# Kernel optimization log

Hardware: AMD Instinct MI355X
Metric: run time of the kernel (lower is better)

## Reference

```python
import jax, jax.numpy as jnp
import numpy as np

N_NODES = 100000
N_EDGES = 3200000
IN_DIM = 256
EMB_DIM = 64
BATCH = 4096
WEIGHT_DECAY = 1e-4


def setup_inputs() -> dict:
    key = jax.random.key(0)
    ks = jax.random.split(key, 8)
    feats = jax.random.normal(ks[0], (N_NODES, IN_DIM), dtype=jnp.float32)
    W = jax.random.normal(ks[1], (IN_DIM, EMB_DIM), dtype=jnp.float32) * (1.0 / np.sqrt(IN_DIM))
    edge_row = jax.random.randint(ks[2], (N_EDGES,), 0, N_NODES, dtype=jnp.int32)
    edge_col = jax.random.randint(ks[3], (N_EDGES,), 0, N_NODES, dtype=jnp.int32)
    edge_val = jax.random.uniform(ks[4], (N_EDGES,), dtype=jnp.float32) * 0.05  # normalized adj weights
    idx1 = jax.random.randint(ks[5], (BATCH,), 0, N_NODES, dtype=jnp.int32)
    idx2 = jax.random.randint(ks[6], (BATCH,), 0, N_NODES, dtype=jnp.int32)
    neg_idx = jax.random.randint(ks[7], (BATCH,), 0, N_NODES, dtype=jnp.int32)
    return {"feats": feats, "W": W, "edge_row": edge_row, "edge_col": edge_col,
            "edge_val": edge_val, "idx1": idx1, "idx2": idx2, "neg_idx": neg_idx}


def reference(feats, W, edge_row, edge_col, edge_val, idx1, idx2, neg_idx):
    # GraphConvolution: tanh( A_sparse @ (X @ W) ), A in COO form
    xw = feats @ W                                              # [N, D]
    msgs = edge_val[:, None] * xw[edge_col]                     # [E, D] gather + scale
    h = jax.ops.segment_sum(msgs, edge_row, num_segments=N_NODES)  # sparse-dense matmul
    h = jnp.tanh(h)
    # tf.nn.l2_normalize(embedding, 1)
    sq = jnp.sum(h * h, axis=1, keepdims=True)
    emb = h * jax.lax.rsqrt(jnp.maximum(sq, 1e-12))             # [N, D]
    # embedding lookups
    o1, o2, on = emb[idx1], emb[idx2], emb[neg_idx]             # [B, D] each
    y_ui = jnp.sum(o1 * o2, axis=1)
    y_uj = jnp.sum(o1 * on, axis=1)
    # BPR loss + weight decay (tf.nn.l2_loss = 0.5*sum(x^2))
    bpr = jnp.sum(-jax.nn.log_sigmoid(y_ui - y_uj))
    loss = (bpr + WEIGHT_DECAY * 0.5 * jnp.sum(emb * emb)) / jnp.float32(BATCH)
    return loss
```

## Files before the change

### kernel.cpp

```cpp
#include <hip/hip_runtime.h>
#include <cmath>

#define N_NODES 100000
#define N_EDGES 3200000
#define IN_DIM 256
#define EMB 64
#define BATCH 4096
#define MWAVES 6250
#define NBUCK 782
#define BROWS 128
#define BSTRIDE 4608
#define PSTRIDE 5504
#define EPB 12544
#define NPA 256

typedef unsigned long long u64;
typedef unsigned int u32;
typedef unsigned short u16;
typedef __attribute__((ext_vector_type(8))) short bf16x8;
typedef __attribute__((ext_vector_type(4))) float f32x4;

__device__ __forceinline__ float wave_sum(float v) {
#pragma unroll
    for (int m = 1; m < 64; m <<= 1) v += __shfl_xor(v, m, 64);
    return v;
}

__device__ __forceinline__ u16 f2bf_rne(float f) {
    u32 u = __float_as_uint(f);
    u32 r = ((u >> 16) & 1u) + 0x7FFFu;
    return (u16)((u + r) >> 16);
}

__device__ __forceinline__ float bf2f(u32 bits16) {
    return __uint_as_float(bits16 << 16);
}

__global__ __launch_bounds__(256) void wpack_kernel(const float* __restrict__ W,
                                                    u16* __restrict__ wpack) {
    const int idx = blockIdx.x * 256 + threadIdx.x;
    const int f = idx >> 6, lane = idx & 63;
    const int kt = f >> 2, nt = f & 3;
    const int k0 = kt * 32 + (lane >> 4) * 8;
    const int n  = nt * 16 + (lane & 15);
    u32 buf[4];
#pragma unroll
    for (int jj = 0; jj < 4; ++jj) {
        u16 lo = f2bf_rne(W[(size_t)(k0 + 2 * jj) * EMB + n]);
        u16 hi = f2bf_rne(W[(size_t)(k0 + 2 * jj + 1) * EMB + n]);
        buf[jj] = (u32)lo | ((u32)hi << 16);
    }
    *(uint4*)&wpack[idx * 8] = *(uint4*)buf;
}

__global__ __launch_bounds__(256) void mfma_gemm_kernel(const float* __restrict__ feats,
                                                        const u16* __restrict__ wpack,
                                                        u16* __restrict__ xwb) {
    __shared__ u16 wlds[32 * 64 * 8];
    const int tid = threadIdx.x;
    for (int idx = tid; idx < 32 * 64; idx += 256)
        *(uint4*)&wlds[idx * 8] = *(const uint4*)&wpack[idx * 8];
    __syncthreads();

    const int wave = tid >> 6, lane = tid & 63;
    const int wid = blockIdx.x * 4 + wave;
    if (wid >= MWAVES) return;
    const int row0 = wid * 16;
    const int arow = row0 + (lane & 15);
    const int kbase = (lane >> 4) * 8;
    const float* fr = feats + (size_t)arow * IN_DIM + kbase;

    float4 av[16];
#pragma unroll
    for (int kt = 0; kt < 8; ++kt) {
        av[2 * kt]     = *(const float4*)(fr + kt * 32);
        av[2 * kt + 1] = *(const float4*)(fr + kt * 32 + 4);
    }

    f32x4 acc[4] = {};
    const u16* wl = &wlds[lane * 8];
#pragma unroll
    for (int kt = 0; kt < 8; ++kt) {
        float4 a0 = av[2 * kt], a1 = av[2 * kt + 1];
        u32 ab[4];
        ab[0] = (u32)f2bf_rne(a0.x) | ((u32)f2bf_rne(a0.y) << 16);
        ab[1] = (u32)f2bf_rne(a0.z) | ((u32)f2bf_rne(a0.w) << 16);
        ab[2] = (u32)f2bf_rne(a1.x) | ((u32)f2bf_rne(a1.y) << 16);
        ab[3] = (u32)f2bf_rne(a1.z) | ((u32)f2bf_rne(a1.w) << 16);
        bf16x8 afrag = *(bf16x8*)ab;
#pragma unroll
        for (int nt = 0; nt < 4; ++nt) {
            bf16x8 bfrag = *(const bf16x8*)&wl[(kt * 4 + nt) * 512];
            acc[nt] = __builtin_amdgcn_mfma_f32_16x16x32_bf16(afrag, bfrag, acc[nt], 0, 0, 0);
        }
    }
    const int rb = row0 + (lane >> 4) * 4;
    const int cb = lane & 15;
#pragma unroll
    for (int nt = 0; nt < 4; ++nt)
#pragma unroll
        for (int r = 0; r < 4; ++r)
            xwb[(size_t)(rb + r) * EMB + nt * 16 + cb] = f2bf_rne(acc[nt][r]);
}

__global__ __launch_bounds__(1024, 4) void passA_kernel(const int* __restrict__ erow,
                                                        const int* __restrict__ ecol,
                                                        const float* __restrict__ eval,
                                                        u32* __restrict__ gcursor,
                                                        u64* __restrict__ sorted) {
    __shared__ u64 stage[EPB];
    __shared__ u32 hist[1024];
    __shared__ u32 harr[1024];
    __shared__ u32 cursor[1024];
    __shared__ u32 gbase[1024];

    const int tid = threadIdx.x;
    const int e0 = blockIdx.x * EPB;
    const int total = min(EPB, N_EDGES - e0);

    hist[tid] = 0;
    __syncthreads();

    u64 ent[13];
#pragma unroll
    for (int j = 0; j < 13; ++j) {
        const int le = j * 1024 + tid;
        if (le < total) {
            const int e = e0 + le;
            const int r = erow[e];
            const int c = ecol[e];
            const u16 vb = f2bf_rne(eval[e]);
            ent[j] = (u64)(u32)r | ((u64)(u32)c << 17) | ((u64)vb << 34);
            atomicAdd(&hist[r >> 7], 1u);
        }
    }
    __syncthreads();

    const u32 h = hist[tid];
    harr[tid] = h;
    __syncthreads();
    for (int off = 1; off < 1024; off <<= 1) {
        u32 x = (tid >= off) ? harr[tid - off] : 0;
        __syncthreads();
        harr[tid] += x;
        __syncthreads();
    }
    const u32 myoff = harr[tid] - h;
    __syncthreads();
    harr[tid] = myoff;
    cursor[tid] = myoff;
    gbase[tid] = h ? atomicAdd(&gcursor[tid], h) : 0u;
    __syncthreads();

#pragma unroll
    for (int j = 0; j < 13; ++j) {
        const int le = j * 1024 + tid;
        if (le < total) {
            const u64 p = ent[j];
            const u32 pos = atomicAdd(&cursor[(int)(p & 0x1FFFFu) >> 7], 1u);
            stage[pos] = p;
        }
    }
    __syncthreads();

    for (int i = tid; i < total; i += 1024) {
        const u64 p = stage[i];
        const int bk = (int)(p & 0x1FFFFu) >> 7;
        const u32 gpos = gbase[bk] + ((u32)i - harr[bk]);
        if (gpos < BSTRIDE) sorted[(size_t)bk * BSTRIDE + gpos] = p;
    }
}

__global__ __launch_bounds__(512, 4) void gather_kernel(const u16* __restrict__ xwb,
                                                        u64* __restrict__ sorted,
                                                        const u32* __restrict__ gcursor,
                                                        float* __restrict__ accumA) {
    __shared__ u32 scoff[PSTRIDE];
    __shared__ u16 sval[PSTRIDE];
    __shared__ u32 rhist[BROWS], roff[BROWS], rcur[BROWS], sc[BROWS];
    __shared__ float part[8];
    const int tid = threadIdx.x, wave = tid >> 6, lane = tid & 63;
    const int b = blockIdx.x;
    u64* gbase = sorted + (size_t)b * BSTRIDE;
    const int cnt = min((int)gcursor[b], BSTRIDE);

    if (tid < BROWS) rhist[tid] = 0;
    __syncthreads();

    u64 ent[9];
    int nloc = 0;
    for (int i = tid; i < cnt; i += 512) {
        u64 p = gbase[i];
        ent[nloc++] = p;
        atomicAdd(&rhist[(int)(p & 127u)], 1u);
    }
    __syncthreads();

    if (tid < BROWS) sc[tid] = (rhist[tid] + 7u) & ~7u;
    __syncthreads();
    for (int off = 1; off < BROWS; off <<= 1) {
        u32 x = (tid < BROWS && tid >= off) ? sc[tid - off] : 0;
        __syncthreads();
        if (tid < BROWS) sc[tid] += x;
        __syncthreads();
    }
    if (tid < BROWS) {
        const u32 r0 = sc[tid] - ((rhist[tid] + 7u) & ~7u);
        roff[tid] = r0;
        rcur[tid] = r0;
    }
    __syncthreads();

    for (int j = 0; j < nloc; ++j) {
        const u64 p = ent[j];
        const u32 pos = atomicAdd(&rcur[(int)(p & 127u)], 1u);
        scoff[pos] = (((u32)(p >> 17)) & 0x1FFFFu) << 7;
        sval[pos]  = (u16)(p >> 34);
    }
    __syncthreads();

    if (tid < BROWS) {
        const int e = roff[tid] + rhist[tid];
        const int pe = roff[tid] + (int)((rhist[tid] + 7u) & ~7u);
        for (int k = e; k < pe; ++k) { scoff[k] = 0u; sval[k] = 0; }
    }
    __syncthreads();

    u16* embp = (u16*)gbase;
    const int g = lane >> 3;
    const int eoff = (lane & 7) * 16;
    const int g0 = g & 1, g1 = (g >> 1) & 1, g2 = (g >> 2) & 1;
    const int el = (lane & 7) * 8 + 4 * g0 + 2 * g1 + g2;
    const char* xwc = (const char*)xwb;
    float wd = 0.f;

#define FMA8(X, V)                                         \
    acc[0] += (V) * __uint_as_float((X).x << 16);          \
    acc[1] += (V) * __uint_as_float((X).x & 0xFFFF0000u);  \
    acc[2] += (V) * __uint_as_float((X).y << 16);          \
    acc[3] += (V) * __uint_as_float((X).y & 0xFFFF0000u);  \
    acc[4] += (V) * __uint_as_float((X).z << 16);          \
    acc[5] += (V) * __uint_as_float((X).z & 0xFFFF0000u);  \
    acc[6] += (V) * __uint_as_float((X).w << 16);          \
    acc[7] += (V) * __uint_as_float((X).w & 0xFFFF0000u);

    for (int rr = 0; rr < 16; ++rr) {
        const int r = wave * 16 + rr;
        const int n8 = (int)((rhist[r] + 7u) & ~7u);
        const int base = (int)roff[r];
        float acc[8] = {0.f, 0.f, 0.f, 0.f, 0.f, 0.f, 0.f, 0.f};

        int j = 0;
        for (; j + 16 <= n8; j += 16) {
            const int i0 = base + j + g;
            const u32 c0 = scoff[i0];
            const u32 c1 = scoff[i0 + 8];
            const float v0 = bf2f(sval[i0]);
            const float v1 = bf2f(sval[i0 + 8]);
            const uint4 x0 = *(const uint4*)(xwc + (c0 + eoff));
            const uint4 x1 = *(const uint4*)(xwc + (c1 + eoff));
            FMA8(x0, v0)
            FMA8(x1, v1)
        }
        if (j < n8) {
            const int i0 = base + j + g;
            const u32 c0 = scoff[i0];
            const float v0 = bf2f(sval[i0]);
            const uint4 x0 = *(const uint4*)(xwc + (c0 + eoff));
            FMA8(x0, v0)
        }

        float k4[4];
#pragma unroll
        for (int i = 0; i < 4; ++i) {
            const float snd = g0 ? acc[i] : acc[i + 4];
            const float kp  = g0 ? acc[i + 4] : acc[i];
            k4[i] = kp + __shfl_xor(snd, 8, 64);
        }
        float k2[2];
#pragma unroll
        for (int i = 0; i < 2; ++i) {
            const float snd = g1 ? k4[i] : k4[i + 2];
            const float kp  = g1 ? k4[i + 2] : k4[i];
            k2[i] = kp + __shfl_xor(snd, 16, 64);
        }
        const float snd = g2 ? k2[0] : k2[1];
        const float kp  = g2 ? k2[1] : k2[0];
        const float s = kp + __shfl_xor(snd, 32, 64);

        const float t = tanhf(s);
        const float sq = wave_sum(t * t);
        const float rn = rsqrtf(fmaxf(sq, 1e-12f));
        if (b * BROWS + r < N_NODES)
            embp[r * EMB + el] = f2bf_rne(t * rn);
        wd += sq / fmaxf(sq, 1e-12f);
    }
#undef FMA8
    if (lane == 0) part[wave] = wd;
    __syncthreads();
    if (tid == 0) {
        float v = 0.f;
#pragma unroll
        for (int w = 0; w < 8; ++w) v += part[w];
        unsafeAtomicAdd(&accumA[b & 255], v);
    }
}

__device__ __forceinline__ float emb_ld(const u64* __restrict__ sorted, int row, int lane) {
    const u16* rp = (const u16*)(sorted + (size_t)(row >> 7) * BSTRIDE) + (row & 127) * EMB;
    return bf2f(rp[lane]);
}

__global__ __launch_bounds__(256) void bpr_kernel(const u64* __restrict__ sorted,
                                                  const int* __restrict__ idx1,
                                                  const int* __restrict__ idx2,
                                                  const int* __restrict__ nidx,
                                                  float* __restrict__ accumB) {
    const int wave = threadIdx.x >> 6, lane = threadIdx.x & 63;
    const int i = blockIdx.x * 4 + wave;
    float o1 = emb_ld(sorted, idx1[i], lane);
    float o2 = emb_ld(sorted, idx2[i], lane);
    float on = emb_ld(sorted, nidx[i], lane);
    float yui = wave_sum(o1 * o2);
    float yuj = wave_sum(o1 * on);
    if (lane == 0) {
        float x = yui - yuj;
        float li = (x > 0.f) ? log1pf(expf(-x)) : (-x + log1pf(expf(x)));
        unsafeAtomicAdd(&accumB[i & 255], li);
    }
}

__global__ __launch_bounds__(64) void finalize_kernel(const float* __restrict__ accumA,
                                                      const float* __restrict__ accumB,
                                                      float* __restrict__ out) {
    const int t = threadIdx.x;
    float wd = 0.f, bp = 0.f;
#pragma unroll
    for (int k = 0; k < 4; ++k) {
        wd += accumA[t + 64 * k];
        bp += accumB[t + 64 * k];
    }
    wd = wave_sum(wd);
    bp = wave_sum(bp);
    if (t == 0) out[0] = (bp + 1e-4f * 0.5f * wd) / (float)BATCH;
}

extern "C" void kernel_launch(void* const* d_in, const int* in_sizes, int n_in,
                              void* d_out, int out_size, void* d_ws, size_t ws_size,
                              hipStream_t stream) {
    const float* feats = (const float*)d_in[0];
    const float* W     = (const float*)d_in[1];
    const int*   erow  = (const int*)d_in[2];
    const int*   ecol  = (const int*)d_in[3];
    const float* eval  = (const float*)d_in[4];
    const int*   idx1  = (const int*)d_in[5];
    const int*   idx2  = (const int*)d_in[6];
    const int*   nidx  = (const int*)d_in[7];
    float* out = (float*)d_out;

    u16*   xwb     = (u16*)d_ws;
    u64*   sorted  = (u64*)(xwb + (size_t)N_NODES * EMB);
    u32*   gcursor = (u32*)(sorted + (size_t)NBUCK * BSTRIDE);
    float* accumA  = (float*)(gcursor + 1024);
    float* accumB  = accumA + 256;
    u16*   wpack   = (u16*)(accumB + 256);

    hipMemsetAsync(gcursor, 0, (1024 + 512) * sizeof(u32), stream);

    wpack_kernel<<<8, 256, 0, stream>>>(W, wpack);
    mfma_gemm_kernel<<<(MWAVES + 3) / 4, 256, 0, stream>>>(feats, wpack, xwb);
    passA_kernel<<<NPA, 1024, 0, stream>>>(erow, ecol, eval, gcursor, sorted);
    gather_kernel<<<NBUCK, 512, 0, stream>>>(xwb, sorted, gcursor, accumA);
    bpr_kernel<<<BATCH / 4, 256, 0, stream>>>(sorted, idx1, idx2, nidx, accumB);
    finalize_kernel<<<1, 64, 0, stream>>>(accumA, accumB, out);
}
```

Measured before the change: 280.1 us.

## Merge edge bucketing and feature GEMM into one launch, fold memset and finalize

Edge bucketing (pass A) and the X@W MFMA GEMM are merged into a single combo kernel: the first blocks bucket edges and the rest run the GEMM, so the two independent stages overlap on the device. Pass A now uses 512-thread blocks handling half as many edges each, with a shuffle-based scan replacing the barrier-heavy LDS scan. The memset is folded into the wpack kernel, and the finalize kernel is replaced by a last-block-done reduction inside the BPR kernel. Together these cut launch count and idle gaps between stages, at the cost of more global atomics on the bucket cursors and a threadfence/counter handshake at the end.

```diff
diff --git a/kernel.cpp b/kernel.cpp
--- a/kernel.cpp
+++ b/kernel.cpp
@@ -11,8 +11,9 @@
 #define BROWS 128
 #define BSTRIDE 4608
 #define PSTRIDE 5504
-#define EPB 12544
-#define NPA 256
+#define EPB 6272
+#define NPA 511
+#define GBLK 782
 
 typedef unsigned long long u64;
 typedef unsigned int u32;
@@ -37,7 +38,11 @@
 }
 
 __global__ __launch_bounds__(256) void wpack_kernel(const float* __restrict__ W,
-                                                    u16* __restrict__ wpack) {
+                                                    u16* __restrict__ wpackp,
+                                                    u32* __restrict__ zbase) {
+    if (blockIdx.x == 0) {
+        for (int i = threadIdx.x; i < 1540; i += 256) zbase[i] = 0u;
+    }
     const int idx = blockIdx.x * 256 + threadIdx.x;
     const int f = idx >> 6, lane = idx & 63;
     const int kt = f >> 2, nt = f & 3;
@@ -50,124 +55,143 @@
         u16 hi = f2bf_rne(W[(size_t)(k0 + 2 * jj + 1) * EMB + n]);
         buf[jj] = (u32)lo | ((u32)hi << 16);
     }
-    *(uint4*)&wpack[idx * 8] = *(uint4*)buf;
-}
-
-__global__ __launch_bounds__(256) void mfma_gemm_kernel(const float* __restrict__ feats,
-                                                        const u16* __restrict__ wpack,
-                                                        u16* __restrict__ xwb) {
-    __shared__ u16 wlds[32 * 64 * 8];
-    const int tid = threadIdx.x;
-    for (int idx = tid; idx < 32 * 64; idx += 256)
-        *(uint4*)&wlds[idx * 8] = *(const uint4*)&wpack[idx * 8];
-    __syncthreads();
-
-    const int wave = tid >> 6, lane = tid & 63;
-    const int wid = blockIdx.x * 4 + wave;
-    if (wid >= MWAVES) return;
-    const int row0 = wid * 16;
-    const int arow = row0 + (lane & 15);
-    const int kbase = (lane >> 4) * 8;
-    const float* fr = feats + (size_t)arow * IN_DIM + kbase;
-
-    float4 av[16];
-#pragma unroll
-    for (int kt = 0; kt < 8; ++kt) {
-        av[2 * kt]     = *(const float4*)(fr + kt * 32);
-        av[2 * kt + 1] = *(const float4*)(fr + kt * 32 + 4);
-    }
-
-    f32x4 acc[4] = {};
-    const u16* wl = &wlds[lane * 8];
-#pragma unroll
-    for (int kt = 0; kt < 8; ++kt) {
-        float4 a0 = av[2 * kt], a1 = av[2 * kt + 1];
-        u32 ab[4];
-        ab[0] = (u32)f2bf_rne(a0.x) | ((u32)f2bf_rne(a0.y) << 16);
-        ab[1] = (u32)f2bf_rne(a0.z) | ((u32)f2bf_rne(a0.w) << 16);
-        ab[2] = (u32)f2bf_rne(a1.x) | ((u32)f2bf_rne(a1.y) << 16);
-        ab[3] = (u32)f2bf_rne(a1.z) | ((u32)f2bf_rne(a1.w) << 16);
-        bf16x8 afrag = *(bf16x8*)ab;
-#pragma unroll
-        for (int nt = 0; nt < 4; ++nt) {
-            bf16x8 bfrag = *(const bf16x8*)&wl[(kt * 4 + nt) * 512];
-            acc[nt] = __builtin_amdgcn_mfma_f32_16x16x32_bf16(afrag, bfrag, acc[nt], 0, 0, 0);
-        }
-    }
-    const int rb = row0 + (lane >> 4) * 4;
-    const int cb = lane & 15;
-#pragma unroll
-    for (int nt = 0; nt < 4; ++nt)
-#pragma unroll
-        for (int r = 0; r < 4; ++r)
-            xwb[(size_t)(rb + r) * EMB + nt * 16 + cb] = f2bf_rne(acc[nt][r]);
-}
-
-__global__ __launch_bounds__(1024, 4) void passA_kernel(const int* __restrict__ erow,
-                                                        const int* __restrict__ ecol,
-                                                        const float* __restrict__ eval,
-                                                        u32* __restrict__ gcursor,
-                                                        u64* __restrict__ sorted) {
-    __shared__ u64 stage[EPB];
-    __shared__ u32 hist[1024];
-    __shared__ u32 harr[1024];
-    __shared__ u32 cursor[1024];
-    __shared__ u32 gbase[1024];
-
-    const int tid = threadIdx.x;
-    const int e0 = blockIdx.x * EPB;
-    const int total = min(EPB, N_EDGES - e0);
-
-    hist[tid] = 0;
-    __syncthreads();
-
-    u64 ent[13];
-#pragma unroll
-    for (int j = 0; j < 13; ++j) {
-        const int le = j * 1024 + tid;
-        if (le < total) {
-            const int e = e0 + le;
-            const int r = erow[e];
-            const int c = ecol[e];
-            const u16 vb = f2bf_rne(eval[e]);
-            ent[j] = (u64)(u32)r | ((u64)(u32)c << 17) | ((u64)vb << 34);
-            atomicAdd(&hist[r >> 7], 1u);
-        }
-    }
-    __syncthreads();
-
-    const u32 h = hist[tid];
-    harr[tid] = h;
-    __syncthreads();
-    for (int off = 1; off < 1024; off <<= 1) {
-        u32 x = (tid >= off) ? harr[tid - off] : 0;
-        __syncthreads();
-        harr[tid] += x;
-        __syncthreads();
-    }
-    const u32 myoff = harr[tid] - h;
-    __syncthreads();
-    harr[tid] = myoff;
-    cursor[tid] = myoff;
-    gbase[tid] = h ? atomicAdd(&gcursor[tid], h) : 0u;
-    __syncthreads();
-
-#pragma unroll
-    for (int j = 0; j < 13; ++j) {
-        const int le = j * 1024 + tid;
-        if (le < total) {
-            const u64 p = ent[j];
-            const u32 pos = atomicAdd(&cursor[(int)(p & 0x1FFFFu) >> 7], 1u);
-            stage[pos] = p;
-        }
-    }
-    __syncthreads();
-
-    for (int i = tid; i < total; i += 1024) {
-        const u64 p = stage[i];
-        const int bk = (int)(p & 0x1FFFFu) >> 7;
-        const u32 gpos = gbase[bk] + ((u32)i - harr[bk]);
-        if (gpos < BSTRIDE) sorted[(size_t)bk * BSTRIDE + gpos] = p;
+    *(uint4*)&wpackp[idx * 8] = *(uint4*)buf;
+}
+
+__global__ __launch_bounds__(512, 4) void combo_kernel(const int* __restrict__ erow,
+                                                       const int* __restrict__ ecol,
+                                                       const float* __restrict__ eval,
+                                                       u32* __restrict__ gcursor,
+                                                       u64* __restrict__ sorted,
+                                                       const float* __restrict__ feats,
+                                                       const u16* __restrict__ wpackp,
+                                                       u16* __restrict__ xwb) {
+    __shared__ union {
+        struct {
+            u64 stage[EPB];
+            u32 hist[1024];
+            u32 cursor[1024];
+            u32 gbase[1024];
+            u32 wsum[8];
+        } pa;
+        u16 wlds[2048 * 8];
+    } sm;
+
+    const int tid = threadIdx.x, wave = tid >> 6, lane = tid & 63;
+    const int bid = blockIdx.x;
+
+    if (bid < NPA) {
+        const int e0 = bid * EPB;
+        const int total = min(EPB, N_EDGES - e0);
+
+        for (int i = tid; i < 1024; i += 512) sm.pa.hist[i] = 0;
+        __syncthreads();
+
+        u64 ent[13];
+#pragma unroll
+        for (int j = 0; j < 13; ++j) {
+            const int le = j * 512 + tid;
+            if (le < total) {
+                const int e = e0 + le;
+                const int r = erow[e];
+                const int c = ecol[e];
+                const u16 vb = f2bf_rne(eval[e]);
+                ent[j] = (u64)(u32)r | ((u64)(u32)c << 17) | ((u64)vb << 34);
+                atomicAdd(&sm.pa.hist[r >> 7], 1u);
+            }
+        }
+        __syncthreads();
+
+        const u32 h0 = sm.pa.hist[tid];
+        const u32 h1 = sm.pa.hist[tid + 512];
+        const u32 s2 = h0 + h1;
+        u32 x = s2;
+#pragma unroll
+        for (int m = 1; m < 64; m <<= 1) {
+            const u32 y = __shfl_up(x, m, 64);
+            if (lane >= m) x += y;
+        }
+        if (lane == 63) sm.pa.wsum[wave] = x;
+        __syncthreads();
+        if (tid < 8) {
+            u32 s = sm.pa.wsum[tid];
+#pragma unroll
+            for (int m = 1; m < 8; m <<= 1) {
+                const u32 y = __shfl_up(s, m, 64);
+                if (tid >= m) s += y;
+            }
+            sm.pa.wsum[tid] = s;
+        }
+        __syncthreads();
+        const u32 base = x - s2 + (wave ? sm.pa.wsum[wave - 1] : 0u);
+        sm.pa.hist[tid]         = base;
+        sm.pa.hist[tid + 512]   = base + h0;
+        sm.pa.cursor[tid]       = base;
+        sm.pa.cursor[tid + 512] = base + h0;
+        sm.pa.gbase[tid]        = h0 ? atomicAdd(&gcursor[tid], h0) : 0u;
+        sm.pa.gbase[tid + 512]  = h1 ? atomicAdd(&gcursor[tid + 512], h1) : 0u;
+        __syncthreads();
+
+#pragma unroll
+        for (int j = 0; j < 13; ++j) {
+            const int le = j * 512 + tid;
+            if (le < total) {
+                const u64 p = ent[j];
+                const u32 pos = atomicAdd(&sm.pa.cursor[(int)(p & 0x1FFFFu) >> 7], 1u);
+                sm.pa.stage[pos] = p;
+            }
+        }
+        __syncthreads();
+
+        for (int i = tid; i < total; i += 512) {
+            const u64 p = sm.pa.stage[i];
+            const int bk = (int)(p & 0x1FFFFu) >> 7;
+            const u32 gpos = sm.pa.gbase[bk] + ((u32)i - sm.pa.hist[bk]);
+            if (gpos < BSTRIDE) sorted[(size_t)bk * BSTRIDE + gpos] = p;
+        }
+    } else {
+        for (int idx = tid; idx < 2048; idx += 512)
+            *(uint4*)&sm.wlds[idx * 8] = *(const uint4*)&wpackp[idx * 8];
+        __syncthreads();
+
+        const int wid = (bid - NPA) * 8 + wave;
+        if (wid >= MWAVES) return;
+        const int row0 = wid * 16;
+        const int arow = row0 + (lane & 15);
+        const int kbase = (lane >> 4) * 8;
+        const float* fr = feats + (size_t)arow * IN_DIM + kbase;
+
+        float4 av[16];
+#pragma unroll
+        for (int kt = 0; kt < 8; ++kt) {
+            av[2 * kt]     = *(const float4*)(fr + kt * 32);
+            av[2 * kt + 1] = *(const float4*)(fr + kt * 32 + 4);
+        }
+
+        f32x4 acc[4] = {};
+        const u16* wl = &sm.wlds[lane * 8];
+#pragma unroll
+        for (int kt = 0; kt < 8; ++kt) {
+            float4 a0 = av[2 * kt], a1 = av[2 * kt + 1];
+            u32 ab[4];
+            ab[0] = (u32)f2bf_rne(a0.x) | ((u32)f2bf_rne(a0.y) << 16);
+            ab[1] = (u32)f2bf_rne(a0.z) | ((u32)f2bf_rne(a0.w) << 16);
+            ab[2] = (u32)f2bf_rne(a1.x) | ((u32)f2bf_rne(a1.y) << 16);
+            ab[3] = (u32)f2bf_rne(a1.z) | ((u32)f2bf_rne(a1.w) << 16);
+            bf16x8 afrag = *(bf16x8*)ab;
+#pragma unroll
+            for (int nt = 0; nt < 4; ++nt) {
+                bf16x8 bfrag = *(const bf16x8*)&wl[(kt * 4 + nt) * 512];
+                acc[nt] = __builtin_amdgcn_mfma_f32_16x16x32_bf16(afrag, bfrag, acc[nt], 0, 0, 0);
+            }
+        }
+        const int rb = row0 + (lane >> 4) * 4;
+        const int cb = lane & 15;
+#pragma unroll
+        for (int nt = 0; nt < 4; ++nt)
+#pragma unroll
+            for (int r = 0; r < 4; ++r)
+                xwb[(size_t)(rb + r) * EMB + nt * 16 + cb] = f2bf_rne(acc[nt][r]);
     }
 }
 
@@ -315,7 +339,11 @@
                                                   const int* __restrict__ idx1,
                                                   const int* __restrict__ idx2,
                                                   const int* __restrict__ nidx,
-                                                  float* __restrict__ accumB) {
+                                                  const float* __restrict__ accumA,
+                                                  float* __restrict__ accumB,
+                                                  u32* __restrict__ donecnt,
+                                                  float* __restrict__ out) {
+    __shared__ u32 lastBlk;
     const int wave = threadIdx.x >> 6, lane = threadIdx.x & 63;
     const int i = blockIdx.x * 4 + wave;
     float o1 = emb_ld(sorted, idx1[i], lane);
@@ -328,21 +356,29 @@
         float li = (x > 0.f) ? log1pf(expf(-x)) : (-x + log1pf(expf(x)));
         unsafeAtomicAdd(&accumB[i & 255], li);
     }
-}
-
-__global__ __launch_bounds__(64) void finalize_kernel(const float* __restrict__ accumA,
-                                                      const float* __restrict__ accumB,
-                                                      float* __restrict__ out) {
-    const int t = threadIdx.x;
-    float wd = 0.f, bp = 0.f;
-#pragma unroll
-    for (int k = 0; k < 4; ++k) {
-        wd += accumA[t + 64 * k];
-        bp += accumB[t + 64 * k];
-    }
-    wd = wave_sum(wd);
-    bp = wave_sum(bp);
-    if (t == 0) out[0] = (bp + 1e-4f * 0.5f * wd) / (float)BATCH;
+    __syncthreads();
+    if (threadIdx.x == 0) {
+        __threadfence();
+        lastBlk = (atomicAdd(donecnt, 1u) == (u32)gridDim.x - 1u) ? 1u : 0u;
+    }
+    __syncthreads();
+    if (lastBlk) {
+        __threadfence();
+        const int t = threadIdx.x;
+        if (t < 64) {
+            const volatile float* vA = accumA;
+            const volatile float* vB = accumB;
+            float wd = 0.f, bp = 0.f;
+#pragma unroll
+            for (int k = 0; k < 4; ++k) {
+                wd += vA[t + 64 * k];
+                bp += vB[t + 64 * k];
+            }
+            wd = wave_sum(wd);
+            bp = wave_sum(bp);
+            if (t == 0) out[0] = (bp + 1e-4f * 0.5f * wd) / (float)BATCH;
+        }
+    }
 }
 
 extern "C" void kernel_launch(void* const* d_in, const int* in_sizes, int n_in,
@@ -363,14 +399,13 @@
     u32*   gcursor = (u32*)(sorted + (size_t)NBUCK * BSTRIDE);
     float* accumA  = (float*)(gcursor + 1024);
     float* accumB  = accumA + 256;
-    u16*   wpack   = (u16*)(accumB + 256);
-
-    hipMemsetAsync(gcursor, 0, (1024 + 512) * sizeof(u32), stream);
-
-    wpack_kernel<<<8, 256, 0, stream>>>(W, wpack);
-    mfma_gemm_kernel<<<(MWAVES + 3) / 4, 256, 0, stream>>>(feats, wpack, xwb);
-    passA_kernel<<<NPA, 1024, 0, stream>>>(erow, ecol, eval, gcursor, sorted);
+    u32*   donecnt = (u32*)(accumB + 256);
+    u16*   wpackp  = (u16*)(donecnt + 4);
+
+    wpack_kernel<<<8, 256, 0, stream>>>(W, wpackp, gcursor);
+    combo_kernel<<<NPA + GBLK, 512, 0, stream>>>(erow, ecol, eval, gcursor, sorted,
+                                                 feats, wpackp, xwb);
     gather_kernel<<<NBUCK, 512, 0, stream>>>(xwb, sorted, gcursor, accumA);
-    bpr_kernel<<<BATCH / 4, 256, 0, stream>>>(sorted, idx1, idx2, nidx, accumB);
-    finalize_kernel<<<1, 64, 0, stream>>>(accumA, accumB, out);
-}
+    bpr_kernel<<<BATCH / 4, 256, 0, stream>>>(sorted, idx1, idx2, nidx,
+                                              accumA, accumB, donecnt, out);
+}
```

After: 293.0 us. 4.6% more time.

## Split sorted edge entries into u32/u16 arrays, fuse memset and finalize

Applied to the files above, without the earlier changes.

Sorted edge records shrink from packed 64-bit words to a 32-bit column+row word plus a separate 16-bit value, so the scatter in passA and the read in gather_kernel move less data. The block-wide Hillis-Steele scan in passA is replaced by a wave-shuffle scan, which needs far fewer barriers. The memset is folded into wpack_kernel, and the finalize kernel is folded into bpr_kernel through a last-block counter, removing two launches. In exchange it adds a threadfence/atomic completion protocol. The embedding buffer now reuses the smaller 32-bit region, which still fits 128 rows of 64 bf16 (4096 u32 per bucket against a stride of 4608).

```diff
diff --git a/kernel.cpp b/kernel.cpp
--- a/kernel.cpp
+++ b/kernel.cpp
@@ -37,7 +37,11 @@
 }
 
 __global__ __launch_bounds__(256) void wpack_kernel(const float* __restrict__ W,
-                                                    u16* __restrict__ wpack) {
+                                                    u16* __restrict__ wpackp,
+                                                    u32* __restrict__ zbase) {
+    if (blockIdx.x == 0) {
+        for (int i = threadIdx.x; i < 1540; i += 256) zbase[i] = 0u;
+    }
     const int idx = blockIdx.x * 256 + threadIdx.x;
     const int f = idx >> 6, lane = idx & 63;
     const int kt = f >> 2, nt = f & 3;
@@ -50,16 +54,16 @@
         u16 hi = f2bf_rne(W[(size_t)(k0 + 2 * jj + 1) * EMB + n]);
         buf[jj] = (u32)lo | ((u32)hi << 16);
     }
-    *(uint4*)&wpack[idx * 8] = *(uint4*)buf;
+    *(uint4*)&wpackp[idx * 8] = *(uint4*)buf;
 }
 
 __global__ __launch_bounds__(256) void mfma_gemm_kernel(const float* __restrict__ feats,
-                                                        const u16* __restrict__ wpack,
+                                                        const u16* __restrict__ wpackp,
                                                         u16* __restrict__ xwb) {
     __shared__ u16 wlds[32 * 64 * 8];
     const int tid = threadIdx.x;
     for (int idx = tid; idx < 32 * 64; idx += 256)
-        *(uint4*)&wlds[idx * 8] = *(const uint4*)&wpack[idx * 8];
+        *(uint4*)&wlds[idx * 8] = *(const uint4*)&wpackp[idx * 8];
     __syncthreads();
 
     const int wave = tid >> 6, lane = tid & 63;
@@ -107,14 +111,15 @@
                                                         const int* __restrict__ ecol,
                                                         const float* __restrict__ eval,
                                                         u32* __restrict__ gcursor,
-                                                        u64* __restrict__ sorted) {
+                                                        u32* __restrict__ centry,
+                                                        u16* __restrict__ ventry) {
     __shared__ u64 stage[EPB];
     __shared__ u32 hist[1024];
-    __shared__ u32 harr[1024];
     __shared__ u32 cursor[1024];
     __shared__ u32 gbase[1024];
-
-    const int tid = threadIdx.x;
+    __shared__ u32 wsum[16];
+
+    const int tid = threadIdx.x, wave = tid >> 6, lane = tid & 63;
     const int e0 = blockIdx.x * EPB;
     const int total = min(EPB, N_EDGES - e0);
 
@@ -137,19 +142,28 @@
     __syncthreads();
 
     const u32 h = hist[tid];
-    harr[tid] = h;
-    __syncthreads();
-    for (int off = 1; off < 1024; off <<= 1) {
-        u32 x = (tid >= off) ? harr[tid - off] : 0;
-        __syncthreads();
-        harr[tid] += x;
-        __syncthreads();
-    }
-    const u32 myoff = harr[tid] - h;
-    __syncthreads();
-    harr[tid] = myoff;
-    cursor[tid] = myoff;
-    gbase[tid] = h ? atomicAdd(&gcursor[tid], h) : 0u;
+    u32 x = h;
+#pragma unroll
+    for (int m = 1; m < 64; m <<= 1) {
+        const u32 y = __shfl_up(x, m, 64);
+        if (lane >= m) x += y;
+    }
+    if (lane == 63) wsum[wave] = x;
+    __syncthreads();
+    if (tid < 16) {
+        u32 s = wsum[tid];
+#pragma unroll
+        for (int m = 1; m < 16; m <<= 1) {
+            const u32 y = __shfl_up(s, m, 16);
+            if (tid >= m) s += y;
+        }
+        wsum[tid] = s;
+    }
+    __syncthreads();
+    const u32 base = x - h + (wave ? wsum[wave - 1] : 0u);
+    hist[tid]   = base;
+    cursor[tid] = base;
+    gbase[tid]  = h ? atomicAdd(&gcursor[tid], h) : 0u;
     __syncthreads();
 
 #pragma unroll
@@ -166,13 +180,18 @@
     for (int i = tid; i < total; i += 1024) {
         const u64 p = stage[i];
         const int bk = (int)(p & 0x1FFFFu) >> 7;
-        const u32 gpos = gbase[bk] + ((u32)i - harr[bk]);
-        if (gpos < BSTRIDE) sorted[(size_t)bk * BSTRIDE + gpos] = p;
+        const u32 gpos = gbase[bk] + ((u32)i - hist[bk]);
+        if (gpos < BSTRIDE) {
+            const size_t o = (size_t)bk * BSTRIDE + gpos;
+            centry[o] = ((((u32)(p >> 17)) & 0x1FFFFu) << 7) | (((u32)p & 127u) << 24);
+            ventry[o] = (u16)(p >> 34);
+        }
     }
 }
 
 __global__ __launch_bounds__(512, 4) void gather_kernel(const u16* __restrict__ xwb,
-                                                        u64* __restrict__ sorted,
+                                                        u32* __restrict__ centry,
+                                                        const u16* __restrict__ ventry,
                                                         const u32* __restrict__ gcursor,
                                                         float* __restrict__ accumA) {
     __shared__ u32 scoff[PSTRIDE];
@@ -181,18 +200,22 @@
     __shared__ float part[8];
     const int tid = threadIdx.x, wave = tid >> 6, lane = tid & 63;
     const int b = blockIdx.x;
-    u64* gbase = sorted + (size_t)b * BSTRIDE;
+    u32* cb_ = centry + (size_t)b * BSTRIDE;
+    const u16* vb_ = ventry + (size_t)b * BSTRIDE;
     const int cnt = min((int)gcursor[b], BSTRIDE);
 
     if (tid < BROWS) rhist[tid] = 0;
     __syncthreads();
 
-    u64 ent[9];
+    u32 cent[9];
+    u16 vent[9];
     int nloc = 0;
     for (int i = tid; i < cnt; i += 512) {
-        u64 p = gbase[i];
-        ent[nloc++] = p;
-        atomicAdd(&rhist[(int)(p & 127u)], 1u);
+        const u32 c = cb_[i];
+        cent[nloc] = c;
+        vent[nloc] = vb_[i];
+        ++nloc;
+        atomicAdd(&rhist[c >> 24], 1u);
     }
     __syncthreads();
 
@@ -212,10 +235,10 @@
     __syncthreads();
 
     for (int j = 0; j < nloc; ++j) {
-        const u64 p = ent[j];
-        const u32 pos = atomicAdd(&rcur[(int)(p & 127u)], 1u);
-        scoff[pos] = (((u32)(p >> 17)) & 0x1FFFFu) << 7;
-        sval[pos]  = (u16)(p >> 34);
+        const u32 c = cent[j];
+        const u32 pos = atomicAdd(&rcur[c >> 24], 1u);
+        scoff[pos] = c & 0xFFFFFFu;
+        sval[pos]  = vent[j];
     }
     __syncthreads();
 
@@ -226,7 +249,7 @@
     }
     __syncthreads();
 
-    u16* embp = (u16*)gbase;
+    u16* embp = (u16*)cb_;
     const int g = lane >> 3;
     const int eoff = (lane & 7) * 16;
     const int g0 = g & 1, g1 = (g >> 1) & 1, g2 = (g >> 2) & 1;
@@ -306,21 +329,25 @@
     }
 }
 
-__device__ __forceinline__ float emb_ld(const u64* __restrict__ sorted, int row, int lane) {
-    const u16* rp = (const u16*)(sorted + (size_t)(row >> 7) * BSTRIDE) + (row & 127) * EMB;
+__device__ __forceinline__ float emb_ld(const u32* __restrict__ centry, int row, int lane) {
+    const u16* rp = (const u16*)(centry + (size_t)(row >> 7) * BSTRIDE) + (row & 127) * EMB;
     return bf2f(rp[lane]);
 }
 
-__global__ __launch_bounds__(256) void bpr_kernel(const u64* __restrict__ sorted,
+__global__ __launch_bounds__(256) void bpr_kernel(const u32* __restrict__ centry,
                                                   const int* __restrict__ idx1,
                                                   const int* __restrict__ idx2,
                                                   const int* __restrict__ nidx,
-                                                  float* __restrict__ accumB) {
+                                                  const float* __restrict__ accumA,
+                                                  float* __restrict__ accumB,
+                                                  u32* __restrict__ donecnt,
+                                                  float* __restrict__ out) {
+    __shared__ u32 lastBlk;
     const int wave = threadIdx.x >> 6, lane = threadIdx.x & 63;
     const int i = blockIdx.x * 4 + wave;
-    float o1 = emb_ld(sorted, idx1[i], lane);
-    float o2 = emb_ld(sorted, idx2[i], lane);
-    float on = emb_ld(sorted, nidx[i], lane);
+    float o1 = emb_ld(centry, idx1[i], lane);
+    float o2 = emb_ld(centry, idx2[i], lane);
+    float on = emb_ld(centry, nidx[i], lane);
     float yui = wave_sum(o1 * o2);
     float yuj = wave_sum(o1 * on);
     if (lane == 0) {
@@ -328,21 +355,29 @@
         float li = (x > 0.f) ? log1pf(expf(-x)) : (-x + log1pf(expf(x)));
         unsafeAtomicAdd(&accumB[i & 255], li);
     }
-}
-
-__global__ __launch_bounds__(64) void finalize_kernel(const float* __restrict__ accumA,
-                                                      const float* __restrict__ accumB,
-                                                      float* __restrict__ out) {
-    const int t = threadIdx.x;
-    float wd = 0.f, bp = 0.f;
-#pragma unroll
-    for (int k = 0; k < 4; ++k) {
-        wd += accumA[t + 64 * k];
-        bp += accumB[t + 64 * k];
-    }
-    wd = wave_sum(wd);
-    bp = wave_sum(bp);
-    if (t == 0) out[0] = (bp + 1e-4f * 0.5f * wd) / (float)BATCH;
+    __syncthreads();
+    if (threadIdx.x == 0) {
+        __threadfence();
+        lastBlk = (atomicAdd(donecnt, 1u) == (u32)gridDim.x - 1u) ? 1u : 0u;
+    }
+    __syncthreads();
+    if (lastBlk) {
+        __threadfence();
+        const int t = threadIdx.x;
+        if (t < 64) {
+            const volatile float* vA = accumA;
+            const volatile float* vB = accumB;
+            float wd = 0.f, bp = 0.f;
+#pragma unroll
+            for (int k = 0; k < 4; ++k) {
+                wd += vA[t + 64 * k];
+                bp += vB[t + 64 * k];
+            }
+            wd = wave_sum(wd);
+            bp = wave_sum(bp);
+            if (t == 0) out[0] = (bp + 1e-4f * 0.5f * wd) / (float)BATCH;
+        }
+    }
 }
 
 extern "C" void kernel_launch(void* const* d_in, const int* in_sizes, int n_in,
@@ -359,18 +394,18 @@
     float* out = (float*)d_out;
 
     u16*   xwb     = (u16*)d_ws;
-    u64*   sorted  = (u64*)(xwb + (size_t)N_NODES * EMB);
-    u32*   gcursor = (u32*)(sorted + (size_t)NBUCK * BSTRIDE);
+    u32*   centry  = (u32*)(xwb + (size_t)N_NODES * EMB);
+    u16*   ventry  = (u16*)(centry + (size_t)NBUCK * BSTRIDE);
+    u32*   gcursor = (u32*)(ventry + (size_t)NBUCK * BSTRIDE);
     float* accumA  = (float*)(gcursor + 1024);
     float* accumB  = accumA + 256;
-    u16*   wpack   = (u16*)(accumB + 256);
-
-    hipMemsetAsync(gcursor, 0, (1024 + 512) * sizeof(u32), stream);
-
-    wpack_kernel<<<8, 256, 0, stream>>>(W, wpack);
-    mfma_gemm_kernel<<<(MWAVES + 3) / 4, 256, 0, stream>>>(feats, wpack, xwb);
-    passA_kernel<<<NPA, 1024, 0, stream>>>(erow, ecol, eval, gcursor, sorted);
-    gather_kernel<<<NBUCK, 512, 0, stream>>>(xwb, sorted, gcursor, accumA);
-    bpr_kernel<<<BATCH / 4, 256, 0, stream>>>(sorted, idx1, idx2, nidx, accumB);
-    finalize_kernel<<<1, 64, 0, stream>>>(accumA, accumB, out);
-}
+    u32*   donecnt = (u32*)(accumB + 256);
+    u16*   wpackp  = (u16*)(donecnt + 4);
+
+    wpack_kernel<<<8, 256, 0, stream>>>(W, wpackp, gcursor);
+    mfma_gemm_kernel<<<(MWAVES + 3) / 4, 256, 0, stream>>>(feats, wpackp, xwb);
+    passA_kernel<<<NPA, 1024, 0, stream>>>(erow, ecol, eval, gcursor, centry, ventry);
+    gather_kernel<<<NBUCK, 512, 0, stream>>>(xwb, centry, ventry, gcursor, accumA);
+    bpr_kernel<<<BATCH / 4, 256, 0, stream>>>(centry, idx1, idx2, nidx,
+                                              accumA, accumB, donecnt, out);
+}
```

New measurement: 297.3 us. 1.06x slower.
